# Kernel optimization log

Measured on AMD Instinct MI355X. Metric: run time of the kernel, lower is better.

## Reference

```python
import jax, jax.numpy as jnp
import numpy as np


def _affine_mats(thetas, lambda1s, lambda2s, H, W):
    # Replicates torch.stack(rows, dim=1) then stack(dim=2): the 'rows' end up as COLUMNS,
    # exactly matching the original module's construction.
    z = jnp.zeros_like(lambda1s)
    o = jnp.ones_like(lambda1s)
    scale = jnp.stack([jnp.stack([lambda1s, z, z], 1),
                       jnp.stack([z, lambda2s, z], 1),
                       jnp.stack([z, z, o], 1)], axis=2)  # [B,3,3]
    th = -thetas
    rot = jnp.stack([jnp.stack([jnp.cos(th), jnp.sin(th), z], 1),
                     jnp.stack([-jnp.sin(th), jnp.cos(th), z], 1),
                     jnp.stack([z, z, o], 1)], axis=2)
    trans = jnp.stack([jnp.stack([o, z, o * W], 1),
                       jnp.stack([z, o, o * H], 1),
                       jnp.stack([z, z, o], 1)], axis=2)
    fw = rot @ trans                       # forward_warp
    fws = scale @ fw                       # forward_warp_scaled
    overall = jnp.linalg.inv(jnp.linalg.inv(fw) @ fws)
    return overall[:, 0:2, :]              # [B,2,3]


def _affine_grid(theta, H, W):
    # torch affine_grid, align_corners=False: normalized pixel-center coords in [-1,1]
    xs = (jnp.arange(W, dtype=theta.dtype) + 0.5) * (2.0 / W) - 1.0
    ys = (jnp.arange(H, dtype=theta.dtype) + 0.5) * (2.0 / H) - 1.0
    X, Y = jnp.meshgrid(xs, ys)                        # [H,W]
    base = jnp.stack([X, Y, jnp.ones_like(X)], -1)     # [H,W,3]
    return jnp.einsum('bij,hwj->bhwi', theta, base)    # [B,H,W,2] (x,y)


def _grid_sample_bilinear_zeros(x, grid):
    # torch grid_sample(mode='bilinear', padding_mode='zeros', align_corners=False)
    B, C, H, W = x.shape
    gx = (grid[..., 0] + 1.0) * (W * 0.5) - 0.5        # [B,H,W] source pixel coords
    gy = (grid[..., 1] + 1.0) * (H * 0.5) - 0.5
    x0 = jnp.floor(gx); y0 = jnp.floor(gy)
    x1 = x0 + 1.0;      y1 = y0 + 1.0
    wx1 = gx - x0; wx0 = 1.0 - wx1
    wy1 = gy - y0; wy0 = 1.0 - wy1
    x0i = x0.astype(jnp.int32); x1i = x1.astype(jnp.int32)
    y0i = y0.astype(jnp.int32); y1i = y1.astype(jnp.int32)
    b_idx = jnp.arange(B)[:, None, None]

    def gather(yi, xi):
        yc = jnp.clip(yi, 0, H - 1)
        xc = jnp.clip(xi, 0, W - 1)
        v = x[b_idx, :, yc, xc]                        # [B,H,W,C]
        m = ((yi >= 0) & (yi < H) & (xi >= 0) & (xi < W)).astype(x.dtype)
        return v * m[..., None]

    out = (gather(y0i, x0i) * (wy0 * wx0)[..., None]
           + gather(y0i, x1i) * (wy0 * wx1)[..., None]
           + gather(y1i, x0i) * (wy1 * wx0)[..., None]
           + gather(y1i, x1i) * (wy1 * wx1)[..., None])  # [B,H,W,C]
    return jnp.transpose(out, (0, 3, 1, 2))            # [B,C,H,W]


def setup_inputs() -> dict:
    key = jax.random.key(0)
    k1, k2, k3, k4 = jax.random.split(key, 4)
    B, C, H, W = 32, 3, 512, 512
    return {
        'x': jax.random.normal(k1, (B, C, H, W), dtype=jnp.float32),
        'thetas': jax.random.normal(k2, (B,), dtype=jnp.float32),
        'lambda1s': jax.random.uniform(k3, (B,), dtype=jnp.float32),
        'lambda2s': jax.random.uniform(k4, (B,), dtype=jnp.float32),
    }


def reference(x, thetas, lambda1s, lambda2s):
    H, W = x.shape[2], x.shape[3]
    theta = _affine_mats(thetas, lambda1s, lambda2s, H, W)   # [B,2,3]
    grid = _affine_grid(theta, H, W)                         # [B,H,W,2]
    return _grid_sample_bilinear_zeros(x, grid).astype(jnp.float32)
```

## Files before the change

### kernel.cpp

```cpp
#include <hip/hip_runtime.h>
#include <math.h>

constexpr int B = 32;
constexpr int C = 3;
constexpr int H = 512;
constexpr int W = 512;
constexpr int HW = H * W;

__global__ void coef_kernel(const float* __restrict__ thetas,
                            const float* __restrict__ l1s,
                            const float* __restrict__ l2s,
                            float* __restrict__ coef) {
    int b = threadIdx.x;
    if (b >= B) return;
    double th = -(double)thetas[b];
    double c = cos(th), s = sin(th);
    double a = 1.0 / (double)l1s[b];
    double d = 1.0 / (double)l2s[b];
    double t00 = a * c * c + d * s * s;
    double t01 = c * s * (d - a);
    double t11 = a * s * s + d * c * c;
    float* cf = coef + b * 8;
    cf[0] = (float)t00;
    cf[1] = (float)t01;
    cf[2] = (float)t01;
    cf[3] = (float)t11;
    cf[4] = 0.0f; cf[5] = 0.0f; cf[6] = 0.0f; cf[7] = 0.0f;
}

__global__ __launch_bounds__(256)
void warp_kernel(const float* __restrict__ x,
                 const float* __restrict__ coef,
                 float* __restrict__ out) {
    const int tid = threadIdx.x;
    const int b  = blockIdx.y;
    const int h  = (blockIdx.x << 1) | (tid >> 7);
    const int w0 = (tid & 127) << 2;

    const float* cf = coef + b * 8;
    const float t00 = cf[0], t01 = cf[1], t10 = cf[2], t11 = cf[3];

    const float Y = ((float)h + 0.5f) * (2.0f / (float)H) - 1.0f;

    float r[C][4];

    const float* __restrict__ base = x + (size_t)b * C * HW;

    #pragma unroll
    for (int j = 0; j < 4; ++j) {
        const float X = ((float)(w0 + j) + 0.5f) * (2.0f / (float)W) - 1.0f;
        const float gridx = t00 * X + t01 * Y;
        const float gridy = t10 * X + t11 * Y;
        const float gx = (gridx + 1.0f) * ((float)W * 0.5f) - 0.5f;
        const float gy = (gridy + 1.0f) * ((float)H * 0.5f) - 0.5f;

        const float x0f = floorf(gx), y0f = floorf(gy);
        const float wx1 = gx - x0f, wx0 = 1.0f - wx1;
        const float wy1 = gy - y0f, wy0 = 1.0f - wy1;

        const int x0 = (int)x0f, y0 = (int)y0f;
        const int x1 = x0 + 1,  y1 = y0 + 1;

        const bool vx0 = ((unsigned)x0 < (unsigned)W);
        const bool vx1 = ((unsigned)x1 < (unsigned)W);
        const bool vy0 = ((unsigned)y0 < (unsigned)H);
        const bool vy1 = ((unsigned)y1 < (unsigned)H);

        const int xc0 = min(max(x0, 0), W - 1);
        const int xc1 = min(max(x1, 0), W - 1);
        const int yc0 = min(max(y0, 0), H - 1);
        const int yc1 = min(max(y1, 0), H - 1);
        const int i00 = yc0 * W + xc0;
        const int i01 = yc0 * W + xc1;
        const int i10 = yc1 * W + xc0;
        const int i11 = yc1 * W + xc1;

        const float w00 = wy0 * wx0, w01 = wy0 * wx1;
        const float w10 = wy1 * wx0, w11 = wy1 * wx1;

        #pragma unroll
        for (int ch = 0; ch < C; ++ch) {
            const float* __restrict__ p = base + ch * HW;
            float v00 = 0.0f, v01 = 0.0f, v10 = 0.0f, v11 = 0.0f;
            if (vy0 && vx0) v00 = p[i00];
            if (vy0 && vx1) v01 = p[i01];
            if (vy1 && vx0) v10 = p[i10];
            if (vy1 && vx1) v11 = p[i11];
            r[ch][j] = v00 * w00 + v01 * w01 + v10 * w10 + v11 * w11;
        }
    }

    const size_t obase = (size_t)b * C * HW + (size_t)h * W + (size_t)w0;
    #pragma unroll
    for (int ch = 0; ch < C; ++ch) {
        float4 v = make_float4(r[ch][0], r[ch][1], r[ch][2], r[ch][3]);
        *reinterpret_cast<float4*>(out + obase + (size_t)ch * HW) = v;
    }
}

extern "C" void kernel_launch(void* const* d_in, const int* in_sizes, int n_in,
                              void* d_out, int out_size, void* d_ws, size_t ws_size,
                              hipStream_t stream) {
    const float* x       = (const float*)d_in[0];
    const float* thetas  = (const float*)d_in[1];
    const float* l1s     = (const float*)d_in[2];
    const float* l2s     = (const float*)d_in[3];
    float* out           = (float*)d_out;
    float* coef          = (float*)d_ws;

    coef_kernel<<<1, 64, 0, stream>>>(thetas, l1s, l2s, coef);
    warp_kernel<<<dim3(H / 2, B), 256, 0, stream>>>(x, coef, out);
}
```

Before: 232.8 us.

## Fuse coefficient kernel into warp kernel and use paired float2 gathers

Removes the separate coefficient-kernel launch by computing the per-batch affine coefficients in thread 0 of each block and sharing them through LDS. Thread-to-pixel mapping changes from four contiguous pixels per thread to lane-strided pixels, so each wavefront handles contiguous columns and writes coalesced scalar stores. Each bilinear row pair is fetched with one float2 load instead of two scalar loads, with edge clamping and selection logic. Blocks skip all loads when no sample falls inside the image. The cost is a __syncthreads and double-precision trig in every block, plus extra selection logic.

```diff
diff --git a/kernel.cpp b/kernel.cpp
--- a/kernel.cpp
+++ b/kernel.cpp
@@ -7,52 +7,47 @@
 constexpr int W = 512;
 constexpr int HW = H * W;
 
-__global__ void coef_kernel(const float* __restrict__ thetas,
-                            const float* __restrict__ l1s,
-                            const float* __restrict__ l2s,
-                            float* __restrict__ coef) {
-    int b = threadIdx.x;
-    if (b >= B) return;
-    double th = -(double)thetas[b];
-    double c = cos(th), s = sin(th);
-    double a = 1.0 / (double)l1s[b];
-    double d = 1.0 / (double)l2s[b];
-    double t00 = a * c * c + d * s * s;
-    double t01 = c * s * (d - a);
-    double t11 = a * s * s + d * c * c;
-    float* cf = coef + b * 8;
-    cf[0] = (float)t00;
-    cf[1] = (float)t01;
-    cf[2] = (float)t01;
-    cf[3] = (float)t11;
-    cf[4] = 0.0f; cf[5] = 0.0f; cf[6] = 0.0f; cf[7] = 0.0f;
-}
-
 __global__ __launch_bounds__(256)
 void warp_kernel(const float* __restrict__ x,
-                 const float* __restrict__ coef,
+                 const float* __restrict__ thetas,
+                 const float* __restrict__ l1s,
+                 const float* __restrict__ l2s,
                  float* __restrict__ out) {
-    const int tid = threadIdx.x;
-    const int b  = blockIdx.y;
-    const int h  = (blockIdx.x << 1) | (tid >> 7);
-    const int w0 = (tid & 127) << 2;
+    const int b = blockIdx.y;
 
-    const float* cf = coef + b * 8;
-    const float t00 = cf[0], t01 = cf[1], t10 = cf[2], t11 = cf[3];
+    __shared__ float sc[4];
+    if (threadIdx.x == 0) {
+        double th = -(double)thetas[b];
+        double c = cos(th), s = sin(th);
+        double a = 1.0 / (double)l1s[b];
+        double d = 1.0 / (double)l2s[b];
+        sc[0] = (float)(a * c * c + d * s * s);
+        sc[1] = (float)(c * s * (d - a));
+        sc[2] = sc[1];
+        sc[3] = (float)(a * s * s + d * c * c);
+    }
+    __syncthreads();
+    const float t00 = sc[0], t01 = sc[1], t10 = sc[2], t11 = sc[3];
+
+    const int tid   = threadIdx.x;
+    const int lane  = tid & 63;
+    const int wv    = tid >> 6;
+    const int h     = (blockIdx.x << 1) | (wv >> 1);
+    const int wbase = (wv & 1) << 8;
 
     const float Y = ((float)h + 0.5f) * (2.0f / (float)H) - 1.0f;
 
-    float r[C][4];
-
-    const float* __restrict__ base = x + (size_t)b * C * HW;
+    int   xb[4], row0[4], row1[4];
+    bool  xeq[4], vx0[4], vx1[4], pr0[4], pr1[4];
+    float w00[4], w01[4], w10[4], w11[4];
+    bool any_valid = false;
 
     #pragma unroll
     for (int j = 0; j < 4; ++j) {
-        const float X = ((float)(w0 + j) + 0.5f) * (2.0f / (float)W) - 1.0f;
-        const float gridx = t00 * X + t01 * Y;
-        const float gridy = t10 * X + t11 * Y;
-        const float gx = (gridx + 1.0f) * ((float)W * 0.5f) - 0.5f;
-        const float gy = (gridy + 1.0f) * ((float)H * 0.5f) - 0.5f;
+        const int w = wbase + (j << 6) + lane;
+        const float X = ((float)w + 0.5f) * (2.0f / (float)W) - 1.0f;
+        const float gx = (t00 * X + t01 * Y + 1.0f) * ((float)W * 0.5f) - 0.5f;
+        const float gy = (t10 * X + t11 * Y + 1.0f) * ((float)H * 0.5f) - 0.5f;
 
         const float x0f = floorf(gx), y0f = floorf(gy);
         const float wx1 = gx - x0f, wx0 = 1.0f - wx1;
@@ -61,53 +56,70 @@
         const int x0 = (int)x0f, y0 = (int)y0f;
         const int x1 = x0 + 1,  y1 = y0 + 1;
 
-        const bool vx0 = ((unsigned)x0 < (unsigned)W);
-        const bool vx1 = ((unsigned)x1 < (unsigned)W);
+        vx0[j] = ((unsigned)x0 < (unsigned)W);
+        vx1[j] = ((unsigned)x1 < (unsigned)W);
         const bool vy0 = ((unsigned)y0 < (unsigned)H);
         const bool vy1 = ((unsigned)y1 < (unsigned)H);
 
-        const int xc0 = min(max(x0, 0), W - 1);
-        const int xc1 = min(max(x1, 0), W - 1);
-        const int yc0 = min(max(y0, 0), H - 1);
-        const int yc1 = min(max(y1, 0), H - 1);
-        const int i00 = yc0 * W + xc0;
-        const int i01 = yc0 * W + xc1;
-        const int i10 = yc1 * W + xc0;
-        const int i11 = yc1 * W + xc1;
+        const int xbj = min(max(x0, 0), W - 2);
+        xb[j]  = xbj;
+        xeq[j] = (x0 == xbj);
+        const bool anyx = vx0[j] || vx1[j];
+        pr0[j] = vy0 && anyx;
+        pr1[j] = vy1 && anyx;
+        any_valid = any_valid || pr0[j] || pr1[j];
 
-        const float w00 = wy0 * wx0, w01 = wy0 * wx1;
-        const float w10 = wy1 * wx0, w11 = wy1 * wx1;
+        row0[j] = min(max(y0, 0), H - 1) * W + xbj;
+        row1[j] = min(max(y1, 0), H - 1) * W + xbj;
 
+        w00[j] = wy0 * wx0; w01[j] = wy0 * wx1;
+        w10[j] = wy1 * wx0; w11[j] = wy1 * wx1;
+    }
+
+    float r[C][4];
+    #pragma unroll
+    for (int ch = 0; ch < C; ++ch)
         #pragma unroll
-        for (int ch = 0; ch < C; ++ch) {
-            const float* __restrict__ p = base + ch * HW;
-            float v00 = 0.0f, v01 = 0.0f, v10 = 0.0f, v11 = 0.0f;
-            if (vy0 && vx0) v00 = p[i00];
-            if (vy0 && vx1) v01 = p[i01];
-            if (vy1 && vx0) v10 = p[i10];
-            if (vy1 && vx1) v11 = p[i11];
-            r[ch][j] = v00 * w00 + v01 * w01 + v10 * w10 + v11 * w11;
+        for (int j = 0; j < 4; ++j) r[ch][j] = 0.0f;
+
+    if (any_valid) {
+        const float* __restrict__ base = x + (size_t)b * C * HW;
+        #pragma unroll
+        for (int j = 0; j < 4; ++j) {
+            #pragma unroll
+            for (int ch = 0; ch < C; ++ch) {
+                const float* __restrict__ p = base + ch * HW;
+                float2 a0 = make_float2(0.0f, 0.0f);
+                float2 a1 = make_float2(0.0f, 0.0f);
+                if (pr0[j]) a0 = *reinterpret_cast<const float2*>(p + row0[j]);
+                if (pr1[j]) a1 = *reinterpret_cast<const float2*>(p + row1[j]);
+                const float v00 = vx0[j] ? (xeq[j] ? a0.x : a0.y) : 0.0f;
+                const float v01 = vx1[j] ? (xeq[j] ? a0.y : a0.x) : 0.0f;
+                const float v10 = vx0[j] ? (xeq[j] ? a1.x : a1.y) : 0.0f;
+                const float v11 = vx1[j] ? (xeq[j] ? a1.y : a1.x) : 0.0f;
+                r[ch][j] = v00 * w00[j] + v01 * w01[j] + v10 * w10[j] + v11 * w11[j];
+            }
         }
     }
 
-    const size_t obase = (size_t)b * C * HW + (size_t)h * W + (size_t)w0;
+    const size_t obase = (size_t)b * C * HW + (size_t)h * W + (size_t)wbase + lane;
     #pragma unroll
     for (int ch = 0; ch < C; ++ch) {
-        float4 v = make_float4(r[ch][0], r[ch][1], r[ch][2], r[ch][3]);
-        *reinterpret_cast<float4*>(out + obase + (size_t)ch * HW) = v;
+        #pragma unroll
+        for (int j = 0; j < 4; ++j) {
+            out[obase + (size_t)ch * HW + (j << 6)] = r[ch][j];
+        }
     }
 }
 
 extern "C" void kernel_launch(void* const* d_in, const int* in_sizes, int n_in,
                               void* d_out, int out_size, void* d_ws, size_t ws_size,
                               hipStream_t stream) {
-    const float* x       = (const float*)d_in[0];
-    const float* thetas  = (const float*)d_in[1];
-    const float* l1s     = (const float*)d_in[2];
-    const float* l2s     = (const float*)d_in[3];
-    float* out           = (float*)d_out;
-    float* coef          = (float*)d_ws;
+    const float* x      = (const float*)d_in[0];
+    const float* thetas = (const float*)d_in[1];
+    const float* l1s    = (const float*)d_in[2];
+    const float* l2s    = (const float*)d_in[3];
+    float* out          = (float*)d_out;
 
-    coef_kernel<<<1, 64, 0, stream>>>(thetas, l1s, l2s, coef);
-    warp_kernel<<<dim3(H / 2, B), 256, 0, stream>>>(x, coef, out);
+    warp_kernel<<<dim3(H / 2, B), 256, 0, stream>>>(x, thetas, l1s, l2s, out);
 }
```

After: 188.2 us. -19.2%, faster.
